# Kernel optimization log

Hardware: AMD Instinct MI355X
Metric: run time of the kernel (lower is better)

## Reference

```python
import jax, jax.numpy as jnp
import numpy as np

EPS = 1e-12


def setup_inputs() -> dict:
    key = jax.random.key(0)
    k = jax.random.split(key, 6)
    B, C, T, A = 8, 1536, 4096, 128
    x = jax.random.normal(k[0], (B, C, T), dtype=jnp.float32)
    lengths = jax.random.randint(k[1], (B,), T // 2, T + 1, dtype=jnp.int64)
    W1 = jax.random.normal(k[2], (A, 3 * C), dtype=jnp.float32) * (1.0 / np.sqrt(3 * C))
    b1 = jax.random.normal(k[3], (A,), dtype=jnp.float32) * 0.01
    W2 = jax.random.normal(k[4], (1, A), dtype=jnp.float32) * (1.0 / np.sqrt(A))
    b2 = jax.random.normal(k[5], (1,), dtype=jnp.float32) * 0.01
    return {"x": x, "lengths": lengths, "W1": W1, "b1": b1, "W2": W2, "b2": b2}


def reference(x, lengths, W1, b1, W2, b2):
    # x: [B, C, T]
    B, C, T = x.shape
    mask = (jnp.arange(T)[None, :] < lengths[:, None]).astype(x.dtype)  # [B, T]
    m3 = mask[:, None, :]  # [B, 1, T]

    # causal (cumulative) mean / std for global context
    count = jnp.clip(jnp.cumsum(mask, axis=1), 1.0)[:, None, :]        # [B, 1, T]
    causal_mean = jnp.cumsum(x * m3, axis=2) / count                   # [B, C, T]
    causal_var = jnp.cumsum(x * x * m3, axis=2) / count - causal_mean ** 2
    causal_std = jnp.sqrt(jnp.clip(causal_var, EPS))

    attn_in = jnp.concatenate([x, causal_mean, causal_std], axis=1)    # [B, 3C, T]
    attn_in = attn_in.transpose(0, 2, 1)                               # [B, T, 3C]

    h = jnp.tanh(attn_in @ W1.T + b1)                                  # [B, T, A]
    logits = (h @ W2.T + b2)[..., 0]                                   # [B, T]

    # logits are query-independent, so causal softmax row q is
    # exp(l_k) / cumsum(exp(l))_q for k <= q -> O(T*C) prefix scan.
    e = jnp.exp(logits - jnp.max(logits, axis=1, keepdims=True))       # [B, T]
    Z = jnp.cumsum(e, axis=1)[:, None, :]                              # [B, 1, T]
    ew = e[:, None, :]                                                 # [B, 1, T]

    weighted_mean = jnp.cumsum(ew * x, axis=2) / Z                     # [B, C, T]
    sq_diff = (x - weighted_mean) ** 2
    weighted_var = jnp.cumsum(ew * sq_diff, axis=2) / Z
    weighted_std = jnp.sqrt(jnp.clip(weighted_var, EPS))

    # each causal softmax row sums to 1 -> final weights are 1/(T+eps)
    fw = 1.0 / (jnp.asarray(T, x.dtype) + EPS)
    final_mean = jnp.sum(weighted_mean, axis=2) * fw                   # [B, C]
    final_std = jnp.sum(weighted_std, axis=2) * fw
    return jnp.concatenate([final_mean, final_std], axis=1)            # [B, 2C]
```

## Files before the change

kernel.cpp:

```cpp
#include <hip/hip_runtime.h>
#include <hip/hip_bf16.h>

#define B_ 8
#define C_ 1536
#define T_ 4096
#define A_ 128
#define K3_ 4608
#define M16_ 256
#define SCW_ 104

typedef _Float16 h8  __attribute__((ext_vector_type(8)));
typedef float    f4  __attribute__((ext_vector_type(4)));

__global__ void k0_pack(const float* __restrict__ W1, _Float16* __restrict__ W1f) {
    int i = blockIdx.x * 256 + threadIdx.x;
    if (i >= A_ * K3_) return;
    int a = i / K3_, k = i - a * K3_;
    int t8 = a >> 4, r15 = a & 15;
    int kb = k >> 5, q = (k >> 3) & 3, j = k & 7;
    int lane = q * 16 + r15;
    W1f[(size_t)((kb * 8 + t8) * 64 + lane) * 8 + j] = (_Float16)W1[i];
}

__global__ __launch_bounds__(256) void k1_carryT(
    const float* __restrict__ x, const int* __restrict__ lens,
    float2* __restrict__ carryT)
{
    const int pid  = blockIdx.x * 4 + (threadIdx.x >> 6);
    const int lane = threadIdx.x & 63;
    const int b    = pid / 768;
    const int c0   = (pid - b * 768) * 2;
    const int len  = lens[b];
    const float* xr0 = x + ((size_t)b * C_ + c0) * T_;
    const float* xr1 = xr0 + T_;
    float2* ct = carryT + (size_t)b * M16_ * C_ + c0;
    const int grp = lane >> 2;
    float bA1 = 0.f, bA2 = 0.f, bB1 = 0.f, bB2 = 0.f;
#pragma unroll
    for (int g = 0; g < 16; ++g) {
        const int t0g = g * 256;
        if (t0g >= len) {
            if ((lane & 3) == 0) {
                float4 st = {bA1, bA2, bB1, bB2};
                *(float4*)&ct[(size_t)(g * 16 + grp) * C_] = st;
            }
            continue;
        }
        float4 va = *(const float4*)(xr0 + t0g + lane * 4);
        float4 vb = *(const float4*)(xr1 + t0g + lane * 4);
        float sA1, sA2, sB1, sB2;
        if (t0g + 256 <= len) {
            sA1 = (va.x + va.y) + (va.z + va.w);
            sA2 = (va.x * va.x + va.y * va.y) + (va.z * va.z + va.w * va.w);
            sB1 = (vb.x + vb.y) + (vb.z + vb.w);
            sB2 = (vb.x * vb.x + vb.y * vb.y) + (vb.z * vb.z + vb.w * vb.w);
        } else {
            const int tbase = t0g + lane * 4;
            float av[4] = {va.x, va.y, va.z, va.w};
            float bv[4] = {vb.x, vb.y, vb.z, vb.w};
            sA1 = sA2 = sB1 = sB2 = 0.f;
#pragma unroll
            for (int j = 0; j < 4; ++j) {
                bool in = (tbase + j) < len;
                float ma = in ? av[j] : 0.f;
                float mb = in ? bv[j] : 0.f;
                sA1 += ma; sA2 += ma * av[j];
                sB1 += mb; sB2 += mb * bv[j];
            }
        }
        sA1 += __shfl_xor(sA1, 1, 64); sA2 += __shfl_xor(sA2, 1, 64);
        sB1 += __shfl_xor(sB1, 1, 64); sB2 += __shfl_xor(sB2, 1, 64);
        sA1 += __shfl_xor(sA1, 2, 64); sA2 += __shfl_xor(sA2, 2, 64);
        sB1 += __shfl_xor(sB1, 2, 64); sB2 += __shfl_xor(sB2, 2, 64);
        float VA1 = sA1, VA2 = sA2, VB1 = sB1, VB2 = sB2;
#pragma unroll
        for (int d = 4; d < 64; d <<= 1) {
            float oA1 = __shfl_up(VA1, d, 64);
            float oA2 = __shfl_up(VA2, d, 64);
            float oB1 = __shfl_up(VB1, d, 64);
            float oB2 = __shfl_up(VB2, d, 64);
            if (lane >= d) { VA1 += oA1; VA2 += oA2; VB1 += oB1; VB2 += oB2; }
        }
        if ((lane & 3) == 0) {
            float4 st = {bA1 + VA1 - sA1, bA2 + VA2 - sA2,
                         bB1 + VB1 - sB1, bB2 + VB2 - sB2};
            *(float4*)&ct[(size_t)(g * 16 + grp) * C_] = st;
        }
        bA1 += __shfl(VA1, 63, 64);
        bA2 += __shfl(VA2, 63, 64);
        bB1 += __shfl(VB1, 63, 64);
        bB2 += __shfl(VB2, 63, 64);
    }
}

__global__ __launch_bounds__(256, 4) void k2h(
    const float* __restrict__ x, const int* __restrict__ lens,
    const float2* __restrict__ carryT, const _Float16* __restrict__ W1f,
    const float* __restrict__ b1, const float* __restrict__ W2,
    float* __restrict__ logits)
{
    __shared__ _Float16 sc_all[4 * 16 * SCW_];
    __shared__ float s_b1[A_], s_w2[A_];

    const int tid = threadIdx.x, lane = tid & 63, w = tid >> 6;
    const int bid = blockIdx.x;
    const int b   = bid >> 6;
    const int t0w = (bid & 63) * 64 + w * 16;
    const int m16 = t0w >> 4;
    const int len = lens[b];
    if (tid < A_) { s_b1[tid] = b1[tid]; s_w2[tid] = W2[tid]; }
    __syncthreads();

    const int kc = lane >> 1;
    const int th = lane & 1;
    const int tb = t0w + th * 8;
    _Float16* sc = sc_all + w * (16 * SCW_);
    const int kcol = (((kc >> 3) ^ (th << 1)) << 3) + (kc & 7);
    _Float16* scw = sc + th * 8 * SCW_ + kcol;
    const h8* W1f8 = (const h8*)W1f;

    const bool beyond = t0w >= len;
    const bool full   = (t0w + 16) <= len;

    float rn_l[8];
#pragma unroll
    for (int j = 0; j < 8; ++j)
        rn_l[j] = __builtin_amdgcn_rcpf((float)min(tb + j + 1, len));

    f4 acc[8] = {};
    const float* xptr = x + ((size_t)b * C_ + kc) * T_ + tb;
    const float2* crp = carryT + ((size_t)b * M16_ + m16) * C_ + kc;

    const int t15 = lane & 15, k8 = lane >> 4;
    const int rdbase = t15 * SCW_ + ((k8 ^ ((t15 >> 3) << 1)) << 3);

    for (int step = 0; step < 48; ++step) {
        float4 xa = ((const float4*)xptr)[0];
        float4 xb = ((const float4*)xptr)[1];
        xptr += 32 * (size_t)T_;
        const float2 cr = crp[(size_t)step * 32];
        float xs[8] = {xa.x, xa.y, xa.z, xa.w, xb.x, xb.y, xb.z, xb.w};

        if (beyond) {
            const float rn0 = rn_l[0];
            const float mn = cr.x * rn0;
            const float sd = sqrtf(fmaxf(cr.y * rn0 - mn * mn, 1e-12f));
            const _Float16 hm = (_Float16)mn, hs = (_Float16)sd;
#pragma unroll
            for (int j = 0; j < 8; ++j) {
                scw[j * SCW_]      = (_Float16)xs[j];
                scw[j * SCW_ + 32] = hm;
                scw[j * SCW_ + 64] = hs;
            }
        } else {
            float ls1 = 0.f, ls2 = 0.f;
            if (full) {
#pragma unroll
                for (int j = 0; j < 8; ++j) { ls1 += xs[j]; ls2 += xs[j] * xs[j]; }
            } else {
#pragma unroll
                for (int j = 0; j < 8; ++j) {
                    float mv = (tb + j < len) ? xs[j] : 0.f;
                    ls1 += mv; ls2 += mv * xs[j];
                }
            }
            const float o1 = __shfl_xor(ls1, 1, 64);
            const float o2 = __shfl_xor(ls2, 1, 64);
            float r1 = cr.x + (th ? o1 : 0.f);
            float r2 = cr.y + (th ? o2 : 0.f);
            if (full) {
#pragma unroll
                for (int j = 0; j < 8; ++j) {
                    const float xval = xs[j];
                    r1 += xval; r2 += xval * xval;
                    const float mn = r1 * rn_l[j];
                    const float sd = sqrtf(fmaxf(r2 * rn_l[j] - mn * mn, 1e-12f));
                    scw[j * SCW_]      = (_Float16)xval;
                    scw[j * SCW_ + 32] = (_Float16)mn;
                    scw[j * SCW_ + 64] = (_Float16)sd;
                }
            } else {
#pragma unroll
                for (int j = 0; j < 8; ++j) {
                    const float xval = xs[j];
                    const float mv = (tb + j < len) ? xval : 0.f;
                    r1 += mv; r2 += mv * xval;
                    const float mn = r1 * rn_l[j];
                    const float sd = sqrtf(fmaxf(r2 * rn_l[j] - mn * mn, 1e-12f));
                    scw[j * SCW_]      = (_Float16)xval;
                    scw[j * SCW_ + 32] = (_Float16)mn;
                    scw[j * SCW_ + 64] = (_Float16)sd;
                }
            }
        }
#pragma unroll
        for (int p = 0; p < 3; ++p) {
            h8 bf = *(const h8*)&sc[rdbase + p * 32];
            const int kb = p * 48 + step;
#pragma unroll
            for (int ii = 0; ii < 8; ++ii) {
                h8 af = W1f8[(size_t)(kb * 8 + ii) * 64 + lane];
                acc[ii] = __builtin_amdgcn_mfma_f32_16x16x32_f16(af, bf, acc[ii], 0, 0, 0);
            }
        }
    }

    const int q = lane >> 4;
    float pr = 0.f;
#pragma unroll
    for (int ii = 0; ii < 8; ++ii)
#pragma unroll
        for (int rg = 0; rg < 4; ++rg) {
            const int a = ii * 16 + q * 4 + rg;
            pr += tanhf(acc[ii][rg] + s_b1[a]) * s_w2[a];
        }
    pr += __shfl_xor(pr, 16, 64);
    pr += __shfl_xor(pr, 32, 64);
    if (lane < 16)
        logits[(size_t)b * T_ + t0w + t15] = pr;
}

__global__ __launch_bounds__(1024) void k3_softmax(
    const float* __restrict__ logits, float* __restrict__ earr,
    float* __restrict__ zarr)
{
    __shared__ float wsum[16];
    const int b = blockIdx.x, tid = threadIdx.x, lane = tid & 63, w = tid >> 6;
    float4 v = *(const float4*)(logits + (size_t)b * T_ + tid * 4);
    float e0 = expf(v.x), e1 = expf(v.y), e2 = expf(v.z), e3 = expf(v.w);
    float s = (e0 + e1) + (e2 + e3);
    float V = s;
#pragma unroll
    for (int d = 1; d < 64; d <<= 1) {
        float o = __shfl_up(V, d, 64);
        if (lane >= d) V += o;
    }
    if (lane == 63) wsum[w] = V;
    __syncthreads();
    float wb = 0.f;
#pragma unroll
    for (int i = 0; i < 16; ++i) wb += (i < w) ? wsum[i] : 0.f;
    float run = wb + (V - s);
    float4 ev, zv;
    ev.x = e0; run += e0; zv.x = run;
    ev.y = e1; run += e1; zv.y = run;
    ev.z = e2; run += e2; zv.z = run;
    ev.w = e3; run += e3; zv.w = run;
    *(float4*)(earr + (size_t)b * T_ + tid * 4) = ev;
    *(float4*)(zarr + (size_t)b * T_ + tid * 4) = zv;
}

__global__ __launch_bounds__(256) void k4_wstats(
    const float* __restrict__ x, const float* __restrict__ earr,
    const float* __restrict__ zarr, float* __restrict__ out)
{
    const int pid  = blockIdx.x * 4 + (threadIdx.x >> 6);
    const int lane = threadIdx.x & 63;
    const int b = pid / 768;
    const int c = (pid - b * 768) * 2;
    const float* xr0 = x + ((size_t)b * C_ + c) * T_;
    const float* xr1 = xr0 + T_;
    const float* er = earr + (size_t)b * T_;
    const float* zr = zarr + (size_t)b * T_;
    float am0 = 0.f, asd0 = 0.f, am1 = 0.f, asd1 = 0.f;
    float bS0 = 0.f, bD0 = 0.f, bS1 = 0.f, bD1 = 0.f;
#pragma unroll 4
    for (int g = 0; g < 16; ++g) {
        const int off = g * 256 + lane * 4;
        float4 ev = *(const float4*)(er + off);
        float4 zv = *(const float4*)(zr + off);
        float4 xa = *(const float4*)(xr0 + off);
        float4 xb = *(const float4*)(xr1 + off);
        float sA0 = ev.x * xa.x;
        float sA1 = sA0 + ev.y * xa.y;
        float sA2 = sA1 + ev.z * xa.z;
        float sA3 = sA2 + ev.w * xa.w;
        float sB0 = ev.x * xb.x;
        float sB1 = sB0 + ev.y * xb.y;
        float sB2 = sB1 + ev.z * xb.z;
        float sB3 = sB2 + ev.w * xb.w;
        float VA = sA3, VB = sB3;
#pragma unroll
        for (int d = 1; d < 64; d <<= 1) {
            float oA = __shfl_up(VA, d, 64);
            float oB = __shfl_up(VB, d, 64);
            if (lane >= d) { VA += oA; VB += oB; }
        }
        const float SxA = bS0 + (VA - sA3);
        const float SxB = bS1 + (VB - sB3);
        bS0 += __shfl(VA, 63, 64);
        bS1 += __shfl(VB, 63, 64);
        const float rz0 = __builtin_amdgcn_rcpf(zv.x);
        const float rz1 = __builtin_amdgcn_rcpf(zv.y);
        const float rz2 = __builtin_amdgcn_rcpf(zv.z);
        const float rz3 = __builtin_amdgcn_rcpf(zv.w);
        const float wmA0 = (SxA + sA0) * rz0, wmA1 = (SxA + sA1) * rz1;
        const float wmA2 = (SxA + sA2) * rz2, wmA3 = (SxA + sA3) * rz3;
        const float wmB0 = (SxB + sB0) * rz0, wmB1 = (SxB + sB1) * rz1;
        const float wmB2 = (SxB + sB2) * rz2, wmB3 = (SxB + sB3) * rz3;
        am0 += (wmA0 + wmA1) + (wmA2 + wmA3);
        am1 += (wmB0 + wmB1) + (wmB2 + wmB3);
        const float dA0 = xa.x - wmA0, dA1 = xa.y - wmA1;
        const float dA2 = xa.z - wmA2, dA3 = xa.w - wmA3;
        const float dB0 = xb.x - wmB0, dB1 = xb.y - wmB1;
        const float dB2 = xb.z - wmB2, dB3 = xb.w - wmB3;
        float qA0 = ev.x * dA0 * dA0;
        float qA1 = qA0 + ev.y * dA1 * dA1;
        float qA2 = qA1 + ev.z * dA2 * dA2;
        float qA3 = qA2 + ev.w * dA3 * dA3;
        float qB0 = ev.x * dB0 * dB0;
        float qB1 = qB0 + ev.y * dB1 * dB1;
        float qB2 = qB1 + ev.z * dB2 * dB2;
        float qB3 = qB2 + ev.w * dB3 * dB3;
        float WA = qA3, WB = qB3;
#pragma unroll
        for (int d = 1; d < 64; d <<= 1) {
            float oA = __shfl_up(WA, d, 64);
            float oB = __shfl_up(WB, d, 64);
            if (lane >= d) { WA += oA; WB += oB; }
        }
        const float DxA = bD0 + (WA - qA3);
        const float DxB = bD1 + (WB - qB3);
        bD0 += __shfl(WA, 63, 64);
        bD1 += __shfl(WB, 63, 64);
        asd0 += (sqrtf(fmaxf((DxA + qA0) * rz0, 1e-12f)) +
                 sqrtf(fmaxf((DxA + qA1) * rz1, 1e-12f))) +
                (sqrtf(fmaxf((DxA + qA2) * rz2, 1e-12f)) +
                 sqrtf(fmaxf((DxA + qA3) * rz3, 1e-12f)));
        asd1 += (sqrtf(fmaxf((DxB + qB0) * rz0, 1e-12f)) +
                 sqrtf(fmaxf((DxB + qB1) * rz1, 1e-12f))) +
                (sqrtf(fmaxf((DxB + qB2) * rz2, 1e-12f)) +
                 sqrtf(fmaxf((DxB + qB3) * rz3, 1e-12f)));
    }
#pragma unroll
    for (int d = 1; d < 64; d <<= 1) {
        am0  += __shfl_xor(am0, d, 64);
        am1  += __shfl_xor(am1, d, 64);
        asd0 += __shfl_xor(asd0, d, 64);
        asd1 += __shfl_xor(asd1, d, 64);
    }
    if (lane == 0) {
        out[(size_t)b * (2 * C_) + c]          = am0  * (1.f / 4096.f);
        out[(size_t)b * (2 * C_) + c + 1]      = am1  * (1.f / 4096.f);
        out[(size_t)b * (2 * C_) + C_ + c]     = asd0 * (1.f / 4096.f);
        out[(size_t)b * (2 * C_) + C_ + c + 1] = asd1 * (1.f / 4096.f);
    }
}

extern "C" void kernel_launch(void* const* d_in, const int* in_sizes, int n_in,
                              void* d_out, int out_size, void* d_ws, size_t ws_size,
                              hipStream_t stream) {
    const float* x    = (const float*)d_in[0];
    const int*   lens = (const int*)d_in[1];
    const float* W1   = (const float*)d_in[2];
    const float* b1   = (const float*)d_in[3];
    const float* W2   = (const float*)d_in[4];
    float* out = (float*)d_out;
    char* ws = (char*)d_ws;

    float2*    carryT = (float2*)ws;
    _Float16*  W1f    = (_Float16*)(ws + 25165824);
    float*     logits = (float*)(ws + 26345472);
    float*     earr   = (float*)(ws + 26476544);
    float*     zarr   = (float*)(ws + 26607616);

    k0_pack   <<<(A_ * K3_ + 255) / 256, 256, 0, stream>>>(W1, W1f);
    k1_carryT <<<(B_ * C_) / 8, 256, 0, stream>>>(x, lens, carryT);
    k2h       <<<B_ * 64, 256, 0, stream>>>(x, lens, carryT, W1f, b1, W2, logits);
    k3_softmax<<<B_, 1024, 0, stream>>>(logits, earr, zarr);
    k4_wstats <<<(B_ * C_) / 8, 256, 0, stream>>>(x, earr, zarr, out);
}
```

Baseline: 527.2 us.

## Retile attention GEMM into 32-timestep blocks with split-K across warps and halved carry table

The logits kernel now gives each block 32 timesteps instead of 64. Its four warps are split into two A-halves by two K-halves, so each warp does 24 K steps over 2 N-tiles × 4 A-tiles instead of 48 steps over 1 × 8. Each W1 fragment loaded from global feeds two MFMAs, roughly halving W1 traffic per timestep. The partial sums from the two K-halves are then reduced through shared memory. The carry table coarsens to 32-timestep granularity, which halves its size and write traffic, and the per-lane reciprocal table is now computed inline. The cost is extra shared-memory reduction, three block barriers and more shared memory per block, which may affect occupancy.

Result: faster. 459.0 us (-12.9%).

```diff
diff --git a/kernel.cpp b/kernel.cpp
--- a/kernel.cpp
+++ b/kernel.cpp
@@ -6,7 +6,7 @@
 #define T_ 4096
 #define A_ 128
 #define K3_ 4608
-#define M16_ 256
+#define M32_ 128
 #define SCW_ 104
 
 typedef _Float16 h8  __attribute__((ext_vector_type(8)));
@@ -33,16 +33,16 @@
     const int len  = lens[b];
     const float* xr0 = x + ((size_t)b * C_ + c0) * T_;
     const float* xr1 = xr0 + T_;
-    float2* ct = carryT + (size_t)b * M16_ * C_ + c0;
-    const int grp = lane >> 2;
+    float2* ct = carryT + (size_t)b * M32_ * C_ + c0;
+    const int grp = lane >> 3;
     float bA1 = 0.f, bA2 = 0.f, bB1 = 0.f, bB2 = 0.f;
 #pragma unroll
     for (int g = 0; g < 16; ++g) {
         const int t0g = g * 256;
         if (t0g >= len) {
-            if ((lane & 3) == 0) {
+            if ((lane & 7) == 0) {
                 float4 st = {bA1, bA2, bB1, bB2};
-                *(float4*)&ct[(size_t)(g * 16 + grp) * C_] = st;
+                *(float4*)&ct[(size_t)(g * 8 + grp) * C_] = st;
             }
             continue;
         }
@@ -72,19 +72,21 @@
         sB1 += __shfl_xor(sB1, 1, 64); sB2 += __shfl_xor(sB2, 1, 64);
         sA1 += __shfl_xor(sA1, 2, 64); sA2 += __shfl_xor(sA2, 2, 64);
         sB1 += __shfl_xor(sB1, 2, 64); sB2 += __shfl_xor(sB2, 2, 64);
+        sA1 += __shfl_xor(sA1, 4, 64); sA2 += __shfl_xor(sA2, 4, 64);
+        sB1 += __shfl_xor(sB1, 4, 64); sB2 += __shfl_xor(sB2, 4, 64);
         float VA1 = sA1, VA2 = sA2, VB1 = sB1, VB2 = sB2;
 #pragma unroll
-        for (int d = 4; d < 64; d <<= 1) {
+        for (int d = 8; d < 64; d <<= 1) {
             float oA1 = __shfl_up(VA1, d, 64);
             float oA2 = __shfl_up(VA2, d, 64);
             float oB1 = __shfl_up(VB1, d, 64);
             float oB2 = __shfl_up(VB2, d, 64);
             if (lane >= d) { VA1 += oA1; VA2 += oA2; VB1 += oB1; VB2 += oB2; }
         }
-        if ((lane & 3) == 0) {
+        if ((lane & 7) == 0) {
             float4 st = {bA1 + VA1 - sA1, bA2 + VA2 - sA2,
                          bB1 + VB1 - sB1, bB2 + VB2 - sB2};
-            *(float4*)&ct[(size_t)(g * 16 + grp) * C_] = st;
+            *(float4*)&ct[(size_t)(g * 8 + grp) * C_] = st;
         }
         bA1 += __shfl(VA1, 63, 64);
         bA2 += __shfl(VA2, 63, 64);
@@ -93,131 +95,148 @@
     }
 }
 
-__global__ __launch_bounds__(256, 4) void k2h(
+__global__ __launch_bounds__(256, 4) void k2i(
     const float* __restrict__ x, const int* __restrict__ lens,
     const float2* __restrict__ carryT, const _Float16* __restrict__ W1f,
     const float* __restrict__ b1, const float* __restrict__ W2,
     float* __restrict__ logits)
 {
-    __shared__ _Float16 sc_all[4 * 16 * SCW_];
+    __shared__ __align__(16) char smem[27648];
     __shared__ float s_b1[A_], s_w2[A_];
+    __shared__ float s_pr[2][32];
 
     const int tid = threadIdx.x, lane = tid & 63, w = tid >> 6;
+    const int ah = w & 1;
+    const int kh = w >> 1;
     const int bid = blockIdx.x;
-    const int b   = bid >> 6;
-    const int t0w = (bid & 63) * 64 + w * 16;
-    const int m16 = t0w >> 4;
+    const int b   = bid >> 7;
+    const int m   = bid & 127;
+    const int t0  = m << 5;
     const int len = lens[b];
     if (tid < A_) { s_b1[tid] = b1[tid]; s_w2[tid] = W2[tid]; }
-    __syncthreads();
 
     const int kc = lane >> 1;
     const int th = lane & 1;
-    const int tb = t0w + th * 8;
-    _Float16* sc = sc_all + w * (16 * SCW_);
+    _Float16* sc = (_Float16*)smem + w * (32 * SCW_);
     const int kcol = (((kc >> 3) ^ (th << 1)) << 3) + (kc & 7);
     _Float16* scw = sc + th * 8 * SCW_ + kcol;
     const h8* W1f8 = (const h8*)W1f;
-
-    const bool beyond = t0w >= len;
-    const bool full   = (t0w + 16) <= len;
-
-    float rn_l[8];
-#pragma unroll
-    for (int j = 0; j < 8; ++j)
-        rn_l[j] = __builtin_amdgcn_rcpf((float)min(tb + j + 1, len));
-
-    f4 acc[8] = {};
-    const float* xptr = x + ((size_t)b * C_ + kc) * T_ + tb;
-    const float2* crp = carryT + ((size_t)b * M16_ + m16) * C_ + kc;
+    const int c_base = kh * 768;
+
+    const bool beyond = t0 >= len;
+    const bool full   = (t0 + 32) <= len;
+
+    f4 acc[2][4] = {};
+    const float* xptr = x + ((size_t)b * C_ + c_base + kc) * T_ + t0 + th * 8;
+    const float2* crp = carryT + ((size_t)b * M32_ + m) * C_ + c_base + kc;
 
     const int t15 = lane & 15, k8 = lane >> 4;
     const int rdbase = t15 * SCW_ + ((k8 ^ ((t15 >> 3) << 1)) << 3);
 
-    for (int step = 0; step < 48; ++step) {
-        float4 xa = ((const float4*)xptr)[0];
-        float4 xb = ((const float4*)xptr)[1];
-        xptr += 32 * (size_t)T_;
+    for (int step = 0; step < 24; ++step) {
         const float2 cr = crp[(size_t)step * 32];
-        float xs[8] = {xa.x, xa.y, xa.z, xa.w, xb.x, xb.y, xb.z, xb.w};
-
-        if (beyond) {
-            const float rn0 = rn_l[0];
-            const float mn = cr.x * rn0;
-            const float sd = sqrtf(fmaxf(cr.y * rn0 - mn * mn, 1e-12f));
-            const _Float16 hm = (_Float16)mn, hs = (_Float16)sd;
-#pragma unroll
-            for (int j = 0; j < 8; ++j) {
-                scw[j * SCW_]      = (_Float16)xs[j];
-                scw[j * SCW_ + 32] = hm;
-                scw[j * SCW_ + 64] = hs;
-            }
-        } else {
-            float ls1 = 0.f, ls2 = 0.f;
-            if (full) {
-#pragma unroll
-                for (int j = 0; j < 8; ++j) { ls1 += xs[j]; ls2 += xs[j] * xs[j]; }
+        float base1 = cr.x, base2 = cr.y;
+#pragma unroll
+        for (int oc = 0; oc < 2; ++oc) {
+            const int tb = t0 + oc * 16 + th * 8;
+            float xs[8];
+            *(float4*)&xs[0] = ((const float4*)(xptr + oc * 16))[0];
+            *(float4*)&xs[4] = ((const float4*)(xptr + oc * 16))[1];
+            _Float16* scwo = scw + oc * 16 * SCW_;
+            if (beyond) {
+                const float rn0 = __builtin_amdgcn_rcpf((float)len);
+                const float mn = base1 * rn0;
+                const float sd = sqrtf(fmaxf(base2 * rn0 - mn * mn, 1e-12f));
+                const _Float16 hm = (_Float16)mn, hs = (_Float16)sd;
+#pragma unroll
+                for (int j = 0; j < 8; ++j) {
+                    scwo[j * SCW_]      = (_Float16)xs[j];
+                    scwo[j * SCW_ + 32] = hm;
+                    scwo[j * SCW_ + 64] = hs;
+                }
             } else {
-#pragma unroll
-                for (int j = 0; j < 8; ++j) {
-                    float mv = (tb + j < len) ? xs[j] : 0.f;
-                    ls1 += mv; ls2 += mv * xs[j];
+                float ls1 = 0.f, ls2 = 0.f;
+                if (full) {
+#pragma unroll
+                    for (int j = 0; j < 8; ++j) { ls1 += xs[j]; ls2 += xs[j] * xs[j]; }
+                } else {
+#pragma unroll
+                    for (int j = 0; j < 8; ++j) {
+                        float mv = (tb + j < len) ? xs[j] : 0.f;
+                        ls1 += mv; ls2 += mv * xs[j];
+                    }
                 }
-            }
-            const float o1 = __shfl_xor(ls1, 1, 64);
-            const float o2 = __shfl_xor(ls2, 1, 64);
-            float r1 = cr.x + (th ? o1 : 0.f);
-            float r2 = cr.y + (th ? o2 : 0.f);
-            if (full) {
+                const float o1 = __shfl_xor(ls1, 1, 64);
+                const float o2 = __shfl_xor(ls2, 1, 64);
+                float r1 = base1 + (th ? o1 : 0.f);
+                float r2 = base2 + (th ? o2 : 0.f);
 #pragma unroll
                 for (int j = 0; j < 8; ++j) {
                     const float xval = xs[j];
-                    r1 += xval; r2 += xval * xval;
-                    const float mn = r1 * rn_l[j];
-                    const float sd = sqrtf(fmaxf(r2 * rn_l[j] - mn * mn, 1e-12f));
-                    scw[j * SCW_]      = (_Float16)xval;
-                    scw[j * SCW_ + 32] = (_Float16)mn;
-                    scw[j * SCW_ + 64] = (_Float16)sd;
+                    const float mv = (full || (tb + j < len)) ? xval : 0.f;
+                    r1 += mv; r2 += mv * xval;
+                    const float rn = __builtin_amdgcn_rcpf((float)min(tb + j + 1, len));
+                    const float mn = r1 * rn;
+                    const float sd = sqrtf(fmaxf(r2 * rn - mn * mn, 1e-12f));
+                    scwo[j * SCW_]      = (_Float16)xval;
+                    scwo[j * SCW_ + 32] = (_Float16)mn;
+                    scwo[j * SCW_ + 64] = (_Float16)sd;
                 }
-            } else {
-#pragma unroll
-                for (int j = 0; j < 8; ++j) {
-                    const float xval = xs[j];
-                    const float mv = (tb + j < len) ? xval : 0.f;
-                    r1 += mv; r2 += mv * xval;
-                    const float mn = r1 * rn_l[j];
-                    const float sd = sqrtf(fmaxf(r2 * rn_l[j] - mn * mn, 1e-12f));
-                    scw[j * SCW_]      = (_Float16)xval;
-                    scw[j * SCW_ + 32] = (_Float16)mn;
-                    scw[j * SCW_ + 64] = (_Float16)sd;
+                base1 += ls1 + o1;
+                base2 += ls2 + o2;
+            }
+        }
+        xptr += 32 * (size_t)T_;
+        const int kb0 = kh * 24 + step;
+#pragma unroll
+        for (int p = 0; p < 3; ++p) {
+            h8 bf0 = *(const h8*)&sc[rdbase + p * 32];
+            h8 bf1 = *(const h8*)&sc[rdbase + 16 * SCW_ + p * 32];
+            const int kb = p * 48 + kb0;
+#pragma unroll
+            for (int ii = 0; ii < 4; ++ii) {
+                h8 af = W1f8[(size_t)(kb * 8 + ah * 4 + ii) * 64 + lane];
+                acc[0][ii] = __builtin_amdgcn_mfma_f32_16x16x32_f16(af, bf0, acc[0][ii], 0, 0, 0);
+                acc[1][ii] = __builtin_amdgcn_mfma_f32_16x16x32_f16(af, bf1, acc[1][ii], 0, 0, 0);
+            }
+        }
+    }
+
+    __syncthreads();
+    float* red = (float*)smem;
+    if (kh == 1) {
+        float* r = red + ah * 2048;
+#pragma unroll
+        for (int nn = 0; nn < 2; ++nn)
+#pragma unroll
+            for (int ii = 0; ii < 4; ++ii)
+#pragma unroll
+                for (int rg = 0; rg < 4; ++rg)
+                    r[((nn * 4 + ii) * 4 + rg) * 64 + lane] = acc[nn][ii][rg];
+    }
+    __syncthreads();
+    if (kh == 0) {
+        float* r = red + ah * 2048;
+        const int q = lane >> 4;
+#pragma unroll
+        for (int nn = 0; nn < 2; ++nn) {
+            float pr = 0.f;
+#pragma unroll
+            for (int ii = 0; ii < 4; ++ii)
+#pragma unroll
+                for (int rg = 0; rg < 4; ++rg) {
+                    float v = acc[nn][ii][rg] + r[((nn * 4 + ii) * 4 + rg) * 64 + lane];
+                    const int a = ah * 64 + ii * 16 + q * 4 + rg;
+                    pr += tanhf(v + s_b1[a]) * s_w2[a];
                 }
-            }
-        }
-#pragma unroll
-        for (int p = 0; p < 3; ++p) {
-            h8 bf = *(const h8*)&sc[rdbase + p * 32];
-            const int kb = p * 48 + step;
-#pragma unroll
-            for (int ii = 0; ii < 8; ++ii) {
-                h8 af = W1f8[(size_t)(kb * 8 + ii) * 64 + lane];
-                acc[ii] = __builtin_amdgcn_mfma_f32_16x16x32_f16(af, bf, acc[ii], 0, 0, 0);
-            }
-        }
-    }
-
-    const int q = lane >> 4;
-    float pr = 0.f;
-#pragma unroll
-    for (int ii = 0; ii < 8; ++ii)
-#pragma unroll
-        for (int rg = 0; rg < 4; ++rg) {
-            const int a = ii * 16 + q * 4 + rg;
-            pr += tanhf(acc[ii][rg] + s_b1[a]) * s_w2[a];
-        }
-    pr += __shfl_xor(pr, 16, 64);
-    pr += __shfl_xor(pr, 32, 64);
-    if (lane < 16)
-        logits[(size_t)b * T_ + t0w + t15] = pr;
+            pr += __shfl_xor(pr, 16, 64);
+            pr += __shfl_xor(pr, 32, 64);
+            if (lane < 16) s_pr[ah][nn * 16 + lane] = pr;
+        }
+    }
+    __syncthreads();
+    if (tid < 32)
+        logits[(size_t)b * T_ + t0 + tid] = s_pr[0][tid] + s_pr[1][tid];
 }
 
 __global__ __launch_bounds__(1024) void k3_softmax(
@@ -359,14 +378,14 @@
     char* ws = (char*)d_ws;
 
     float2*    carryT = (float2*)ws;
-    _Float16*  W1f    = (_Float16*)(ws + 25165824);
-    float*     logits = (float*)(ws + 26345472);
-    float*     earr   = (float*)(ws + 26476544);
-    float*     zarr   = (float*)(ws + 26607616);
+    _Float16*  W1f    = (_Float16*)(ws + 12582912);
+    float*     logits = (float*)(ws + 13762560);
+    float*     earr   = (float*)(ws + 13893632);
+    float*     zarr   = (float*)(ws + 14024704);
 
     k0_pack   <<<(A_ * K3_ + 255) / 256, 256, 0, stream>>>(W1, W1f);
     k1_carryT <<<(B_ * C_) / 8, 256, 0, stream>>>(x, lens, carryT);
-    k2h       <<<B_ * 64, 256, 0, stream>>>(x, lens, carryT, W1f, b1, W2, logits);
+    k2i       <<<B_ * M32_, 256, 0, stream>>>(x, lens, carryT, W1f, b1, W2, logits);
     k3_softmax<<<B_, 1024, 0, stream>>>(logits, earr, zarr);
     k4_wstats <<<(B_ * C_) / 8, 256, 0, stream>>>(x, earr, zarr, out);
 }
```
